# Kernel optimization log

Hardware: AMD Instinct MI355X
Metric: run time of the kernel (lower is better)

Reference implementation:

```python
import jax, jax.numpy as jnp
import numpy as np

H = 32        # num heads
NOPE = 128    # qk_nope_head_dim
ROPE = 64     # qk_rope_head_dim
VD = 128      # v_head_dim
QL = 1536     # q_lora_rank
KVL = 512     # kv_lora_rank
HID = 4096
S = 2048
EPS = 1e-6
THETA = 10000.0
SCALE = (NOPE + ROPE) ** -0.5


def rmsnorm(x, g, eps=EPS):
    return x * jax.lax.rsqrt(jnp.mean(x * x, axis=-1, keepdims=True) + eps) * g


def apply_rope(x, pos):
    # is_neox_style=False: rotate interleaved even/odd pairs
    d = x.shape[-1]
    inv_freq = 1.0 / (THETA ** (jnp.arange(0, d, 2, dtype=jnp.float32) / d))
    ang = pos.astype(jnp.float32)[:, None] * inv_freq  # [S, d/2]
    cos, sin = jnp.cos(ang), jnp.sin(ang)
    if x.ndim == 3:  # [S, H, d]
        cos, sin = cos[:, None, :], sin[:, None, :]
    x1, x2 = x[..., 0::2], x[..., 1::2]
    o1 = x1 * cos - x2 * sin
    o2 = x2 * cos + x1 * sin
    return jnp.stack([o1, o2], axis=-1).reshape(x.shape)


def setup_inputs() -> dict:
    key = jax.random.key(0)
    ks = jax.random.split(key, 6)
    return {
        "hidden_states": jax.random.normal(ks[0], (S, HID), jnp.float32),
        "w_a": jax.random.normal(ks[1], (HID, QL + KVL + ROPE), jnp.float32) * 0.02,
        "g_qa": jnp.ones((QL,), jnp.float32),
        "w_qb": jax.random.normal(ks[2], (QL, H * (NOPE + ROPE)), jnp.float32) * 0.02,
        "g_kva": jnp.ones((KVL,), jnp.float32),
        "w_kvb": jax.random.normal(ks[3], (KVL, H * (NOPE + VD)), jnp.float32) * 0.02,
        "w_o": jax.random.normal(ks[4], (H * VD, HID), jnp.float32) * 0.02,
        "positions": jnp.arange(S, dtype=jnp.int64),
    }


def reference(hidden_states, w_a, g_qa, w_qb, g_kva, w_kvb, w_o, positions):
    # fused qkv_a projection with MQA latent
    qkv = hidden_states @ w_a                      # [S, QL+KVL+ROPE]
    q_a = qkv[:, :QL]
    kv_a = qkv[:, QL:QL + KVL]
    k_pe = qkv[:, QL + KVL:]                       # [S, ROPE]

    # q path: rmsnorm -> q_b_proj -> split nope/rope
    q = (rmsnorm(q_a, g_qa) @ w_qb).reshape(S, H, NOPE + ROPE)
    q_nope, q_pe = q[..., :NOPE], q[..., NOPE:]
    q_pe = apply_rope(q_pe, positions)             # [S, H, ROPE]

    # latent kv (MQA, single kv head)
    kv_lat = rmsnorm(kv_a, g_kva)                  # [S, KVL]
    k_pe = apply_rope(k_pe, positions)             # [S, ROPE]

    # weight absorption: split kv_b into w_kc / w_vc
    w = w_kvb.reshape(KVL, H, NOPE + VD)
    w_kc = jnp.transpose(w[..., :NOPE], (1, 2, 0))  # [H, NOPE, KVL]
    w_vc = jnp.transpose(w[..., NOPE:], (1, 0, 2))  # [H, KVL, VD]

    # absorb q_nope into latent space
    q_lat = jnp.einsum('shn,hnc->shc', q_nope, w_kc)  # [S, H, KVL]

    # MQA attention over latent KV (shared across heads)
    scores = (jnp.einsum('shc,tc->hst', q_lat, kv_lat)
              + jnp.einsum('shr,tr->hst', q_pe, k_pe)) * SCALE  # [H, S, S]
    causal = positions[:, None] >= positions[None, :]
    scores = jnp.where(causal[None], scores, jnp.finfo(scores.dtype).min)
    probs = jax.nn.softmax(scores, axis=-1)

    o_lat = jnp.einsum('hst,tc->shc', probs, kv_lat)          # [S, H, KVL]
    o = jnp.einsum('shc,hcv->shv', o_lat, w_vc)               # [S, H, VD]
    return o.reshape(S, H * VD) @ w_o                          # [S, HID]
```

## Files before the change

### kernel.cpp

```cpp
#include <hip/hip_runtime.h>
#include <cstdint>
#include <cstddef>

using ushort = unsigned short;
using bf16x8 = __attribute__((ext_vector_type(8))) short;
using f32x4  = __attribute__((ext_vector_type(4))) float;

#define S_    2048
#define HID_  4096
#define QL_   1536
#define KVL_  512
#define ROPE_ 64
#define NH_   32
constexpr float SCALE_ = 0.07216878364870322f;
constexpr float EPS_   = 1e-6f;

__device__ __forceinline__ float bf2f(ushort u){
  union { uint32_t i; float f; } v; v.i = ((uint32_t)u) << 16; return v.f;
}
__device__ __forceinline__ ushort f2bf(float f){
  union { uint32_t i; float f; } v; v.f = f;
  uint32_t r = v.i + 0x7FFFu + ((v.i >> 16) & 1u);
  return (ushort)(r >> 16);
}
__device__ __forceinline__ void gload_lds16(const void* g, void* l){
  __builtin_amdgcn_global_load_lds((const __attribute__((address_space(1))) void*)g,
                                   (__attribute__((address_space(3))) void*)l, 16, 0, 0);
}

__global__ __launch_bounds__(256) void convert_bf16(const float* __restrict__ in,
                                                    ushort* __restrict__ out, size_t n4){
  size_t i = (size_t)blockIdx.x * 256 + threadIdx.x;
  if (i < n4){
    float4 v = ((const float4*)in)[i];
    ushort4 o; o.x = f2bf(v.x); o.y = f2bf(v.y); o.z = f2bf(v.z); o.w = f2bf(v.w);
    ((ushort4*)out)[i] = o;
  }
}

__global__ __launch_bounds__(256) void transpose_cvt(const float* __restrict__ in,
                                                     ushort* __restrict__ out,
                                                     int K, int N, int ldo){
  __shared__ float t[32][33];
  int k0 = blockIdx.x * 32, n0 = blockIdx.y * 32;
  int tx = threadIdx.x & 31, ty = threadIdx.x >> 5;
  #pragma unroll
  for (int i = ty; i < 32; i += 8){
    int k = k0 + i, n = n0 + tx;
    t[i][tx] = (k < K && n < N) ? in[(size_t)k * N + n] : 0.f;
  }
  __syncthreads();
  #pragma unroll
  for (int i = ty; i < 32; i += 8){
    int n = n0 + i, k = k0 + tx;
    if (n < N && k < K) out[(size_t)n * ldo + k] = f2bf(t[tx][i]);
  }
}

template<typename OutT>
__global__ __launch_bounds__(256, 2)
void gemm_bt(const ushort* __restrict__ A, const ushort* __restrict__ B,
             OutT* __restrict__ C, int M, int N, int K,
             int lda, int ldb, int ldc, ushort* __restrict__ vtout){
  __shared__ ushort As[128 * 32];
  __shared__ ushort Bs[128 * 32];
  int tid = threadIdx.x, wave = tid >> 6, lane = tid & 63;
  int m0 = blockIdx.x * 128, n0 = blockIdx.y * 128;
  int wr = wave >> 1, wc = wave & 1;
  f32x4 acc[4][4];
  #pragma unroll
  for (int i = 0; i < 4; i++) for (int j = 0; j < 4; j++) for (int q = 0; q < 4; q++) acc[i][j][q] = 0.f;

  int srow = tid >> 2, skq = (tid & 3) * 8;
  const ushort* gA0 = A + (size_t)(m0 + srow) * lda + skq;
  const ushort* gA1 = A + (size_t)(m0 + 64 + srow) * lda + skq;
  const ushort* gB0 = B + (size_t)(n0 + srow) * ldb + skq;
  const ushort* gB1 = B + (size_t)(n0 + 64 + srow) * ldb + skq;
  char* lA = (char*)As + wave * 1024;
  char* lB = (char*)Bs + wave * 1024;
  int rr = lane & 15, kq = (lane >> 4) * 8;

  int nk = K / 32;
  for (int kt = 0; kt < nk; ++kt){
    __syncthreads();
    gload_lds16(gA0, lA); gload_lds16(gA1, lA + 4096);
    gload_lds16(gB0, lB); gload_lds16(gB1, lB + 4096);
    gA0 += 32; gA1 += 32; gB0 += 32; gB1 += 32;
    __syncthreads();
    bf16x8 af[4], bg[4];
    #pragma unroll
    for (int i = 0; i < 4; i++) af[i] = *(const bf16x8*)&As[(wr * 64 + i * 16 + rr) * 32 + kq];
    #pragma unroll
    for (int j = 0; j < 4; j++) bg[j] = *(const bf16x8*)&Bs[(wc * 64 + j * 16 + rr) * 32 + kq];
    #pragma unroll
    for (int i = 0; i < 4; i++)
      #pragma unroll
      for (int j = 0; j < 4; j++)
        acc[i][j] = __builtin_amdgcn_mfma_f32_16x16x32_bf16(af[i], bg[j], acc[i][j], 0, 0, 0);
  }
  #pragma unroll
  for (int i = 0; i < 4; i++)
    #pragma unroll
    for (int j = 0; j < 4; j++){
      int r0 = m0 + wr * 64 + i * 16 + (lane >> 4) * 4;
      int c0 = n0 + wc * 64 + j * 16 + rr;
      if (c0 < N){
        #pragma unroll
        for (int q = 0; q < 4; q++){
          float v = acc[i][j][q];
          if constexpr (sizeof(OutT) == 2) C[(size_t)(r0 + q) * ldc + c0] = (OutT)f2bf(v);
          else                             C[(size_t)(r0 + q) * ldc + c0] = (OutT)v;
        }
        if (vtout){
          int hh = c0 >> 8, jj = c0 & 255;
          if (jj >= 128){
            short4 pk;
            pk.x = (short)f2bf(acc[i][j][0]); pk.y = (short)f2bf(acc[i][j][1]);
            pk.z = (short)f2bf(acc[i][j][2]); pk.w = (short)f2bf(acc[i][j][3]);
            *(short4*)&vtout[(size_t)(hh * 128 + (jj - 128)) * 2048 + r0] = pk;
          }
        }
      }
    }
}

__global__ __launch_bounds__(256) void norm_rope(const float* __restrict__ qkv,
                                                 const float* __restrict__ gqa,
                                                 const float* __restrict__ gkva,
                                                 ushort* __restrict__ qa_n,
                                                 ushort* __restrict__ kvlat,
                                                 ushort* __restrict__ kpe){
  int s = blockIdx.x, tid = threadIdx.x;
  const float* row = qkv + (size_t)s * 2112;
  __shared__ float red[4];
  __shared__ float bc[2];
  float ss = 0.f;
  for (int j = tid; j < 1536; j += 256){ float v = row[j]; ss += v * v; }
  #pragma unroll
  for (int m = 1; m < 64; m <<= 1) ss += __shfl_xor(ss, m);
  if ((tid & 63) == 0) red[tid >> 6] = ss;
  __syncthreads();
  if (tid == 0) bc[0] = rsqrtf((red[0] + red[1] + red[2] + red[3]) / 1536.f + EPS_);
  float s2 = 0.f;
  for (int j = tid; j < 512; j += 256){ float v = row[1536 + j]; s2 += v * v; }
  #pragma unroll
  for (int m = 1; m < 64; m <<= 1) s2 += __shfl_xor(s2, m);
  __syncthreads();
  if ((tid & 63) == 0) red[tid >> 6] = s2;
  __syncthreads();
  if (tid == 0) bc[1] = rsqrtf((red[0] + red[1] + red[2] + red[3]) / 512.f + EPS_);
  __syncthreads();
  float r1 = bc[0], r2 = bc[1];
  for (int j = tid; j < 1536; j += 256) qa_n[(size_t)s * 1536 + j] = f2bf(row[j] * r1 * gqa[j]);
  for (int j = tid; j < 512;  j += 256) kvlat[(size_t)s * 512 + j] = f2bf(row[1536 + j] * r2 * gkva[j]);
  if (tid < 32){
    int i = tid;
    float inv = powf(10000.f, -(float)i / 32.f);
    float an = (float)s * inv;
    float c = cosf(an), sn = sinf(an);
    float x1 = row[2048 + 2 * i], x2 = row[2048 + 2 * i + 1];
    kpe[(size_t)s * 64 + 2 * i]     = f2bf(x1 * c - x2 * sn);
    kpe[(size_t)s * 64 + 2 * i + 1] = f2bf(x2 * c + x1 * sn);
  }
}

__global__ __launch_bounds__(256) void rope_q(ushort* __restrict__ q){
  int s = blockIdx.x, tid = threadIdx.x;
  int i = tid & 31;
  float inv = powf(10000.f, -(float)i / 32.f);
  float an = (float)s * inv;
  float c = cosf(an), sn = sinf(an);
  for (int h = tid >> 5; h < 32; h += 8){
    size_t b = (size_t)s * 6144 + h * 192 + 128 + 2 * i;
    float x1 = bf2f(q[b]), x2 = bf2f(q[b + 1]);
    q[b]     = f2bf(x1 * c - x2 * sn);
    q[b + 1] = f2bf(x2 * c + x1 * sn);
  }
}

__global__ __launch_bounds__(256, 3)
void flash_attn(const ushort* __restrict__ q, const ushort* __restrict__ ckv,
                const ushort* __restrict__ kpe, const ushort* __restrict__ vT,
                ushort* __restrict__ obuf){
  __shared__ ushort Ks[64][200];
  __shared__ ushort VTs[128][72];
  __shared__ ushort Ps[64][72];
  int h = blockIdx.y;
  int tid = threadIdx.x, wave = tid >> 6, lane = tid & 63;
  int rr = lane & 15, g = lane >> 4, kq = g * 8;
  const ushort* vTh = vT + (size_t)h * 128 * 2048;

  for (int half = 0; half < 2; ++half){
    int qt = half ? 31 - (int)blockIdx.x : (int)blockIdx.x;
    int s0 = qt * 64;
    bf16x8 qf[6];
    const ushort* qrow = q + (size_t)(s0 + wave * 16 + rr) * 6144 + h * 192;
    #pragma unroll
    for (int ks = 0; ks < 6; ks++) qf[ks] = *(const bf16x8*)(qrow + ks * 32 + kq);

    float m_[4], l_[4]; f32x4 oacc[8];
    #pragma unroll
    for (int i = 0; i < 4; i++){ m_[i] = -3e38f; l_[i] = 0.f; }
    #pragma unroll
    for (int v = 0; v < 8; v++) for (int i = 0; i < 4; i++) oacc[v][i] = 0.f;

    for (int kt = 0; kt <= qt; ++kt){
      int t0 = kt * 64;
      __syncthreads();
      for (int c = tid; c < 1536; c += 256){
        int t = c / 24, ch = c % 24;
        bf16x8 val;
        if (ch < 16) val = *(const bf16x8*)&ckv[(size_t)(t0 + t) * 8192 + h * 256 + ch * 8];
        else         val = *(const bf16x8*)&kpe[(size_t)(t0 + t) * 64 + (ch - 16) * 8];
        *(bf16x8*)&Ks[t][ch * 8] = val;
      }
      for (int c = tid; c < 1024; c += 256){
        int v = c >> 3, tc = c & 7;
        *(bf16x8*)&VTs[v][tc * 8] = *(const bf16x8*)&vTh[(size_t)v * 2048 + t0 + tc * 8];
      }
      __syncthreads();

      f32x4 sc[4];
      #pragma unroll
      for (int nt = 0; nt < 4; nt++) for (int i2 = 0; i2 < 4; i2++) sc[nt][i2] = 0.f;
      #pragma unroll
      for (int ks = 0; ks < 6; ks++){
        #pragma unroll
        for (int nt = 0; nt < 4; nt++){
          bf16x8 kf = *(const bf16x8*)&Ks[nt * 16 + rr][ks * 32 + kq];
          sc[nt] = __builtin_amdgcn_mfma_f32_16x16x32_bf16(qf[ks], kf, sc[nt], 0, 0, 0);
        }
      }
      float sv[4][4], mt[4];
      #pragma unroll
      for (int i2 = 0; i2 < 4; i2++) mt[i2] = -3e38f;
      #pragma unroll
      for (int nt = 0; nt < 4; nt++)
        #pragma unroll
        for (int q2 = 0; q2 < 4; q2++){
          float v = sc[nt][q2] * SCALE_;
          if (kt == qt){
            int rowg = s0 + wave * 16 + g * 4 + q2;
            int colg = t0 + nt * 16 + rr;
            if (colg > rowg) v = -3e38f;
          }
          sv[nt][q2] = v;
          mt[q2] = fmaxf(mt[q2], v);
        }
      #pragma unroll
      for (int msk = 1; msk < 16; msk <<= 1)
        #pragma unroll
        for (int q2 = 0; q2 < 4; q2++) mt[q2] = fmaxf(mt[q2], __shfl_xor(mt[q2], msk));
      float f[4], psum[4];
      #pragma unroll
      for (int q2 = 0; q2 < 4; q2++){
        float mn = fmaxf(m_[q2], mt[q2]);
        f[q2] = __expf(m_[q2] - mn);
        m_[q2] = mn;
        psum[q2] = 0.f;
      }
      #pragma unroll
      for (int nt = 0; nt < 4; nt++)
        #pragma unroll
        for (int q2 = 0; q2 < 4; q2++){
          float p = __expf(sv[nt][q2] - m_[q2]);
          psum[q2] += p;
          Ps[wave * 16 + g * 4 + q2][nt * 16 + rr] = f2bf(p);
        }
      #pragma unroll
      for (int msk = 1; msk < 16; msk <<= 1)
        #pragma unroll
        for (int q2 = 0; q2 < 4; q2++) psum[q2] += __shfl_xor(psum[q2], msk);
      #pragma unroll
      for (int q2 = 0; q2 < 4; q2++) l_[q2] = l_[q2] * f[q2] + psum[q2];
      #pragma unroll
      for (int v = 0; v < 8; v++)
        #pragma unroll
        for (int q2 = 0; q2 < 4; q2++) oacc[v][q2] *= f[q2];
      #pragma unroll
      for (int ks = 0; ks < 2; ks++){
        bf16x8 pa = *(const bf16x8*)&Ps[wave * 16 + rr][ks * 32 + kq];
        #pragma unroll
        for (int vt = 0; vt < 8; vt++){
          bf16x8 vb = *(const bf16x8*)&VTs[vt * 16 + rr][ks * 32 + kq];
          oacc[vt] = __builtin_amdgcn_mfma_f32_16x16x32_bf16(pa, vb, oacc[vt], 0, 0, 0);
        }
      }
    }
    #pragma unroll
    for (int vt = 0; vt < 8; vt++)
      #pragma unroll
      for (int q2 = 0; q2 < 4; q2++){
        float v = oacc[vt][q2] / l_[q2];
        obuf[(size_t)(s0 + wave * 16 + g * 4 + q2) * 4096 + h * 128 + vt * 16 + rr] = f2bf(v);
      }
  }
}

extern "C" void kernel_launch(void* const* d_in, const int* in_sizes, int n_in,
                              void* d_out, int out_size, void* d_ws, size_t ws_size,
                              hipStream_t stream){
  (void)in_sizes; (void)n_in; (void)out_size;
  const float* hidden = (const float*)d_in[0];
  const float* w_a    = (const float*)d_in[1];
  const float* g_qa   = (const float*)d_in[2];
  const float* w_qb   = (const float*)d_in[3];
  const float* g_kva  = (const float*)d_in[4];
  const float* w_kvb  = (const float*)d_in[5];
  const float* w_o    = (const float*)d_in[6];
  float* out = (float*)d_out;

  char* base = (char*)d_ws;
  size_t off = 0;
  auto take = [&](size_t b) -> char* { char* p = base + off; off += (b + 255) & ~(size_t)255; return p; };
  ushort* arenaW = (ushort*)take(33554432);
  ushort* arenaB = (ushort*)take(33554432);
  char*   arenaC = take((size_t)S_ * 2112 * 4);
  ushort* qa_n   = (ushort*)take((size_t)S_ * QL_ * 2);
  ushort* qbuf   = (ushort*)take((size_t)S_ * 6144 * 2);
  ushort* kvlat  = (ushort*)take((size_t)S_ * KVL_ * 2);
  ushort* kpe    = (ushort*)take((size_t)S_ * ROPE_ * 2);
  if (off > ws_size) return;

  ushort* hb   = arenaB;
  ushort* ckv  = arenaB;
  float*  qkv  = (float*)arenaC;
  ushort* obuf = (ushort*)arenaC;
  ushort* vT   = arenaW + 8u * 1024 * 1024;

  convert_bf16 <<<8192, 256, 0, stream>>>(hidden, hb, (size_t)S_ * HID_ / 4);
  transpose_cvt<<<dim3(128, 66), 256, 0, stream>>>(w_a, arenaW, 4096, 2112, 4096);
  gemm_bt<float><<<dim3(16, 17), 256, 0, stream>>>(hb, arenaW, qkv, 2048, 2112, 4096, 4096, 4096, 2112, nullptr);
  norm_rope    <<<2048, 256, 0, stream>>>(qkv, g_qa, g_kva, qa_n, kvlat, kpe);
  transpose_cvt<<<dim3(48, 192), 256, 0, stream>>>(w_qb, arenaW, 1536, 6144, 1536);
  gemm_bt<ushort><<<dim3(16, 48), 256, 0, stream>>>(qa_n, arenaW, qbuf, 2048, 6144, 1536, 1536, 1536, 6144, nullptr);
  rope_q       <<<2048, 256, 0, stream>>>(qbuf);
  transpose_cvt<<<dim3(16, 256), 256, 0, stream>>>(w_kvb, arenaW, 512, 8192, 512);
  gemm_bt<ushort><<<dim3(16, 64), 256, 0, stream>>>(kvlat, arenaW, ckv, 2048, 8192, 512, 512, 512, 8192, vT);
  flash_attn   <<<dim3(16, 32), 256, 0, stream>>>(qbuf, ckv, kpe, vT, obuf);
  transpose_cvt<<<dim3(128, 128), 256, 0, stream>>>(w_o, arenaW, 4096, 4096, 4096);
  gemm_bt<float><<<dim3(16, 32), 256, 0, stream>>>(obuf, arenaW, out, 2048, 4096, 4096, 4096, 4096, 4096, nullptr);
}
```

Before: 725.7 us.

## Load K and V fragments directly from global memory in flash attention

The shared-memory staging of K (latent plus rope) and V-transposed tiles is removed, along with the two block-wide barriers per key tile. Each wave now reads its MFMA operands straight from global memory, relying on L2/L1 caching. The P scratch is made per-wave, which shrinks LDS use, and the launch-bounds occupancy hint is dropped. Setprio hints are placed around the MFMA loops. The trade-off is that the four waves no longer share K/V loads, so each tile is fetched from global memory once per wave, with uncoalesced-ish 16-byte row accesses and global memory latency exposed directly before each MFMA.

```diff
diff --git a/kernel.cpp b/kernel.cpp
--- a/kernel.cpp
+++ b/kernel.cpp
@@ -178,17 +178,16 @@
   }
 }
 
-__global__ __launch_bounds__(256, 3)
+__global__ __launch_bounds__(256)
 void flash_attn(const ushort* __restrict__ q, const ushort* __restrict__ ckv,
                 const ushort* __restrict__ kpe, const ushort* __restrict__ vT,
                 ushort* __restrict__ obuf){
-  __shared__ ushort Ks[64][200];
-  __shared__ ushort VTs[128][72];
-  __shared__ ushort Ps[64][72];
+  __shared__ ushort Ps[4][16][72];
   int h = blockIdx.y;
   int tid = threadIdx.x, wave = tid >> 6, lane = tid & 63;
   int rr = lane & 15, g = lane >> 4, kq = g * 8;
   const ushort* vTh = vT + (size_t)h * 128 * 2048;
+  ushort (*ps)[72] = Ps[wave];
 
   for (int half = 0; half < 2; ++half){
     int qt = half ? 31 - (int)blockIdx.x : (int)blockIdx.x;
@@ -206,31 +205,31 @@
 
     for (int kt = 0; kt <= qt; ++kt){
       int t0 = kt * 64;
-      __syncthreads();
-      for (int c = tid; c < 1536; c += 256){
-        int t = c / 24, ch = c % 24;
-        bf16x8 val;
-        if (ch < 16) val = *(const bf16x8*)&ckv[(size_t)(t0 + t) * 8192 + h * 256 + ch * 8];
-        else         val = *(const bf16x8*)&kpe[(size_t)(t0 + t) * 64 + (ch - 16) * 8];
-        *(bf16x8*)&Ks[t][ch * 8] = val;
-      }
-      for (int c = tid; c < 1024; c += 256){
-        int v = c >> 3, tc = c & 7;
-        *(bf16x8*)&VTs[v][tc * 8] = *(const bf16x8*)&vTh[(size_t)v * 2048 + t0 + tc * 8];
-      }
-      __syncthreads();
+      const ushort* kbase = ckv + (size_t)t0 * 8192 + h * 256 + kq;
+      const ushort* pbase = kpe + (size_t)t0 * 64 + kq;
 
       f32x4 sc[4];
       #pragma unroll
       for (int nt = 0; nt < 4; nt++) for (int i2 = 0; i2 < 4; i2++) sc[nt][i2] = 0.f;
-      #pragma unroll
-      for (int ks = 0; ks < 6; ks++){
-        #pragma unroll
-        for (int nt = 0; nt < 4; nt++){
-          bf16x8 kf = *(const bf16x8*)&Ks[nt * 16 + rr][ks * 32 + kq];
+      __builtin_amdgcn_s_setprio(1);
+      #pragma unroll
+      for (int nt = 0; nt < 4; nt++){
+        int trow = nt * 16 + rr;
+        const ushort* kr = kbase + (size_t)trow * 8192;
+        #pragma unroll
+        for (int ks = 0; ks < 4; ks++){
+          bf16x8 kf = *(const bf16x8*)(kr + ks * 32);
           sc[nt] = __builtin_amdgcn_mfma_f32_16x16x32_bf16(qf[ks], kf, sc[nt], 0, 0, 0);
         }
-      }
+        const ushort* pr = pbase + (size_t)trow * 64;
+        #pragma unroll
+        for (int ks = 0; ks < 2; ks++){
+          bf16x8 kf = *(const bf16x8*)(pr + ks * 32);
+          sc[nt] = __builtin_amdgcn_mfma_f32_16x16x32_bf16(qf[4 + ks], kf, sc[nt], 0, 0, 0);
+        }
+      }
+      __builtin_amdgcn_s_setprio(0);
+
       float sv[4][4], mt[4];
       #pragma unroll
       for (int i2 = 0; i2 < 4; i2++) mt[i2] = -3e38f;
@@ -265,7 +264,7 @@
         for (int q2 = 0; q2 < 4; q2++){
           float p = __expf(sv[nt][q2] - m_[q2]);
           psum[q2] += p;
-          Ps[wave * 16 + g * 4 + q2][nt * 16 + rr] = f2bf(p);
+          ps[g * 4 + q2][nt * 16 + rr] = f2bf(p);
         }
       #pragma unroll
       for (int msk = 1; msk < 16; msk <<= 1)
@@ -277,15 +276,18 @@
       for (int v = 0; v < 8; v++)
         #pragma unroll
         for (int q2 = 0; q2 < 4; q2++) oacc[v][q2] *= f[q2];
+
+      __builtin_amdgcn_s_setprio(1);
       #pragma unroll
       for (int ks = 0; ks < 2; ks++){
-        bf16x8 pa = *(const bf16x8*)&Ps[wave * 16 + rr][ks * 32 + kq];
+        bf16x8 pa = *(const bf16x8*)&ps[rr][ks * 32 + kq];
         #pragma unroll
         for (int vt = 0; vt < 8; vt++){
-          bf16x8 vb = *(const bf16x8*)&VTs[vt * 16 + rr][ks * 32 + kq];
+          bf16x8 vb = *(const bf16x8*)&vTh[(size_t)(vt * 16 + rr) * 2048 + t0 + ks * 32 + kq];
           oacc[vt] = __builtin_amdgcn_mfma_f32_16x16x32_bf16(pa, vb, oacc[vt], 0, 0, 0);
         }
       }
+      __builtin_amdgcn_s_setprio(0);
     }
     #pragma unroll
     for (int vt = 0; vt < 8; vt++)
```

Measured after the change: 831.2 us. 1.15x slower.
